# Performance work log

Hardware: AMD Instinct MI355X
Metric: run time of the kernel (lower is better)

## Reference

```python
import jax, jax.numpy as jnp
import numpy as np

N = 50000
E = 800000
D = 128
L = 2


def setup_inputs() -> dict:
    key = jax.random.key(0)
    ks = jax.random.split(key, 8)
    x = jax.random.normal(ks[0], (N, D), dtype=jnp.float32)
    edge_index = jax.random.randint(ks[1], (2, E), 0, N, dtype=jnp.int64)
    s = 1.0 / np.sqrt(D)
    Wl = jax.random.uniform(ks[2], (L, D, D), jnp.float32, -s, s)  # neighbor transform (with bias)
    bl = jax.random.uniform(ks[3], (L, D), jnp.float32, -s, s)
    Wr = jax.random.uniform(ks[4], (L, D, D), jnp.float32, -s, s)  # root/self transform (no bias)
    W = jax.random.uniform(ks[5], (D, D), jnp.float32, -s, s)      # final Linear
    b = jax.random.uniform(ks[6], (D,), jnp.float32, -s, s)
    return {"x": x, "edge_index": edge_index, "Wl": Wl, "bl": bl, "Wr": Wr, "W": W, "b": b}


def reference(x, edge_index, Wl, bl, Wr, W, b):
    src, dst = edge_index[0], edge_index[1]
    n = x.shape[0]
    for l in range(Wl.shape[0]):
        # gather neighbor (source) features, scatter-max into destination nodes
        agg = jax.ops.segment_max(x[src], dst, num_segments=n)  # [N, D]
        agg = jnp.where(jnp.isneginf(agg), 0.0, agg)  # PyG: isolated nodes -> 0
        # SAGEConv: lin_l(agg) + lin_r(x)
        x = agg @ Wl[l].T + bl[l] + x @ Wr[l].T
        x = jax.nn.relu(x)
    return x @ W.T + b
```

## Files before the change

kernel.cpp:

```cpp
#include <hip/hip_runtime.h>
#include <math.h>

#define NN 50000
#define NE 800000
#define DD 128
#define NBUCK 196
#define EPB 2048
#define PB 391
#define CONVB 6250
#define NTILE 782

typedef unsigned short u16;
typedef unsigned long long u64t;
typedef short s8v __attribute__((ext_vector_type(8)));
typedef float f16v __attribute__((ext_vector_type(16)));

__device__ __forceinline__ u16 f2bf(float f) {
    unsigned u = __float_as_uint(f);
    return (u16)((u + 0x7FFFu + ((u >> 16) & 1u)) >> 16);
}
__device__ __forceinline__ float bflo(unsigned u) { return __uint_as_float(u << 16); }
__device__ __forceinline__ float bfhi(unsigned u) { return __uint_as_float(u & 0xFFFF0000u); }

__global__ __launch_bounds__(256) void zero_kernel(int* __restrict__ p, int n) {
    int i = threadIdx.x + blockIdx.x * 256;
    if (i < n) p[i] = 0;
}

__device__ __forceinline__ void pack_one(const float* __restrict__ Wl,
                                         const float* __restrict__ Wr,
                                         bool two, int o, u16* __restrict__ out) {
    int j = o & 7;
    int l = (o >> 3) & 63;
    int cn = o >> 9;
    int n = cn & 3;
    int c = cn >> 2;
    int colj = n * 32 + (l & 31);
    int k = c * 16 + (l >> 5) * 8 + j;
    float v;
    if (two) v = (k < DD) ? Wl[colj * DD + k] : Wr[colj * DD + (k - DD)];
    else     v = Wl[colj * DD + k];
    out[o] = f2bf(v);
}

__global__ __launch_bounds__(256) void prep_kernel(
        const float4* __restrict__ x4, ushort4* __restrict__ hb0,
        ushort4* __restrict__ hbT,
        const float* __restrict__ Wl, const float* __restrict__ Wr,
        const float* __restrict__ W,
        u16* __restrict__ Bpk0, u16* __restrict__ Bpk1, u16* __restrict__ Bpkf,
        const int* __restrict__ ei, int* __restrict__ bcnt) {
    int bid = blockIdx.x;
    int tid = threadIdx.x;
    if (bid < CONVB) {
        int i = bid * 256 + tid;
        float4 v = x4[i];
        ushort4 o;
        o.x = f2bf(v.x); o.y = f2bf(v.y); o.z = f2bf(v.z); o.w = f2bf(v.w);
        hb0[i] = o;
        int node = i >> 5, pos = i & 31;
        hbT[((size_t)((pos >> 3) * NN + node) << 3) + (pos & 7)] = o;
    } else if (bid < CONVB + 128) {
        pack_one(Wl, Wr, true, (bid - CONVB) * 256 + tid, Bpk0);
    } else if (bid < CONVB + 256) {
        pack_one(Wl + DD * DD, Wr + DD * DD, true, (bid - CONVB - 128) * 256 + tid, Bpk1);
    } else if (bid < CONVB + 320) {
        pack_one(W, W, false, (bid - CONVB - 256) * 256 + tid, Bpkf);
    } else {
        __shared__ int h[NBUCK];
        for (int i = tid; i < NBUCK; i += 256) h[i] = 0;
        __syncthreads();
        int e0 = (bid - (CONVB + 320)) * EPB;
#pragma unroll
        for (int i = 0; i < 8; i++) {
            int e = e0 + i * 256 + tid;
            if (e < NE) atomicAdd(&h[ei[NE + e] >> 8], 1);
        }
        __syncthreads();
        for (int i = tid; i < NBUCK; i += 256)
            if (h[i]) atomicAdd(&bcnt[i], h[i]);
    }
}

__global__ __launch_bounds__(256) void bucket_partition(const int* __restrict__ ei,
                                                        const int* __restrict__ bcnt,
                                                        int* __restrict__ claim,
                                                        unsigned* __restrict__ packed,
                                                        int* __restrict__ rowptr) {
    __shared__ int sc[256];
    __shared__ int bb[NBUCK];
    __shared__ int h[NBUCK];
    __shared__ int base[NBUCK];
    int t = threadIdx.x;
    int v = (t < NBUCK) ? bcnt[t] : 0;
    sc[t] = v;
    __syncthreads();
    for (int o = 1; o < 256; o <<= 1) {
        int u = (t >= o) ? sc[t - o] : 0;
        __syncthreads();
        sc[t] += u;
        __syncthreads();
    }
    if (t < NBUCK) bb[t] = sc[t] - v;
    if (t == 0 && blockIdx.x == 0) rowptr[NN] = NE;
    for (int i = t; i < NBUCK; i += 256) h[i] = 0;
    __syncthreads();
    int e0 = blockIdx.x * EPB;
    int dsts[8], srcs[8];
#pragma unroll
    for (int i = 0; i < 8; i++) {
        int e = e0 + i * 256 + t;
        if (e < NE) {
            dsts[i] = ei[NE + e];
            srcs[i] = ei[e];
            atomicAdd(&h[dsts[i] >> 8], 1);
        } else dsts[i] = -1;
    }
    __syncthreads();
    for (int i = t; i < NBUCK; i += 256) {
        int c = h[i];
        base[i] = c ? bb[i] + atomicAdd(&claim[i], c) : 0;
    }
    __syncthreads();
    for (int i = t; i < NBUCK; i += 256) h[i] = 0;
    __syncthreads();
#pragma unroll
    for (int i = 0; i < 8; i++) {
        if (dsts[i] >= 0) {
            int bk = dsts[i] >> 8;
            int r = atomicAdd(&h[bk], 1);
            packed[base[bk] + r] = (unsigned)srcs[i] | ((unsigned)(dsts[i] & 255) << 16);
        }
    }
}

__global__ __launch_bounds__(256) void bucket_csr(const unsigned* __restrict__ packed,
                                                  const int* __restrict__ bcnt,
                                                  int* __restrict__ rowptr,
                                                  int* __restrict__ col) {
    __shared__ int sc[256];
    __shared__ int deg[256];
    __shared__ int off[256];
    int t = threadIdx.x;
    int v0 = (t < NBUCK) ? bcnt[t] : 0;
    sc[t] = v0;
    __syncthreads();
    for (int o = 1; o < 256; o <<= 1) {
        int u = (t >= o) ? sc[t - o] : 0;
        __syncthreads();
        sc[t] += u;
        __syncthreads();
    }
    int bk = blockIdx.x;
    int cnt = bcnt[bk];
    int base = sc[bk] - cnt;
    deg[t] = 0;
    __syncthreads();
    for (int i = t; i < cnt; i += 256) atomicAdd(&deg[packed[base + i] >> 16], 1);
    __syncthreads();
    int v = deg[t];
    off[t] = v;
    __syncthreads();
    for (int o = 1; o < 256; o <<= 1) {
        int u = (t >= o) ? off[t - o] : 0;
        __syncthreads();
        off[t] += u;
        __syncthreads();
    }
    int ex = off[t] - v;
    int node = (bk << 8) + t;
    if (node < NN) rowptr[node] = base + ex;
    deg[t] = ex;
    __syncthreads();
    for (int i = t; i < cnt; i += 256) {
        unsigned p = packed[base + i];
        int dl = p >> 16;
        int r = atomicAdd(&deg[dl], 1);
        col[base + r] = (int)(p & 0xFFFFu);
    }
}

__device__ __forceinline__ void vmax8(float* m, uint4 v) {
    m[0] = fmaxf(m[0], bflo(v.x)); m[1] = fmaxf(m[1], bfhi(v.x));
    m[2] = fmaxf(m[2], bflo(v.y)); m[3] = fmaxf(m[3], bfhi(v.y));
    m[4] = fmaxf(m[4], bflo(v.z)); m[5] = fmaxf(m[5], bfhi(v.z));
    m[6] = fmaxf(m[6], bflo(v.w)); m[7] = fmaxf(m[7], bfhi(v.w));
}

__global__ __launch_bounds__(256) void agg_chunked(const uint4* __restrict__ hbT4,
                                                   const int* __restrict__ rowptr,
                                                   const int* __restrict__ col,
                                                   uint4* __restrict__ aggb4) {
    int bid = blockIdx.x;
    int chunk = (bid & 7) >> 1;
    int ntile = ((bid >> 3) << 1) | (bid & 1);
    int t = threadIdx.x;
    int node = ntile * 64 + (t >> 2);
    int q = t & 3;
    if (node >= NN) return;
    const uint4* src4 = hbT4 + ((size_t)chunk * NN) * 4 + q;
    int s0 = rowptr[node], s1 = rowptr[node + 1];
    uint4 o = make_uint4(0u, 0u, 0u, 0u);
    if (s0 < s1) {
        float m0[8], m1[8];
#pragma unroll
        for (int k = 0; k < 8; k++) { m0[k] = m1[k] = -INFINITY; }
        int i = s0;
        for (; i + 8 <= s1; i += 8) {
            int c0 = col[i],     c1 = col[i + 1], c2 = col[i + 2], c3 = col[i + 3];
            int c4 = col[i + 4], c5 = col[i + 5], c6 = col[i + 6], c7 = col[i + 7];
            uint4 v0 = src4[(size_t)c0 * 4];
            uint4 v1 = src4[(size_t)c1 * 4];
            uint4 v2 = src4[(size_t)c2 * 4];
            uint4 v3 = src4[(size_t)c3 * 4];
            uint4 v4 = src4[(size_t)c4 * 4];
            uint4 v5 = src4[(size_t)c5 * 4];
            uint4 v6 = src4[(size_t)c6 * 4];
            uint4 v7 = src4[(size_t)c7 * 4];
            vmax8(m0, v0); vmax8(m1, v1); vmax8(m0, v2); vmax8(m1, v3);
            vmax8(m0, v4); vmax8(m1, v5); vmax8(m0, v6); vmax8(m1, v7);
        }
        for (; i + 2 <= s1; i += 2) {
            int c0 = col[i], c1 = col[i + 1];
            uint4 v0 = src4[(size_t)c0 * 4];
            uint4 v1 = src4[(size_t)c1 * 4];
            vmax8(m0, v0); vmax8(m1, v1);
        }
        if (i < s1) {
            uint4 v = src4[(size_t)col[i] * 4];
            vmax8(m0, v);
        }
#pragma unroll
        for (int k = 0; k < 8; k++) m0[k] = fmaxf(m0[k], m1[k]);
        o.x = (__float_as_uint(m0[0]) >> 16) | (__float_as_uint(m0[1]) & 0xFFFF0000u);
        o.y = (__float_as_uint(m0[2]) >> 16) | (__float_as_uint(m0[3]) & 0xFFFF0000u);
        o.z = (__float_as_uint(m0[4]) >> 16) | (__float_as_uint(m0[5]) & 0xFFFF0000u);
        o.w = (__float_as_uint(m0[6]) >> 16) | (__float_as_uint(m0[7]) & 0xFFFF0000u);
    }
    aggb4[(size_t)node * 16 + chunk * 4 + q] = o;
}

__global__ __launch_bounds__(256) void mfma_gemm0(const u16* __restrict__ srcA,
                                                  const u16* __restrict__ srcB,
                                                  const u16* __restrict__ Bpk,
                                                  const float* __restrict__ bias,
                                                  u16* __restrict__ outh,
                                                  u16* __restrict__ outT) {
    __shared__ u16 As[128 * 128];
    char* Ab = (char*)As;
    int tid = threadIdx.x;
    int wt = tid >> 6;
    int lane = tid & 63;
    int row0 = blockIdx.x * 128;
    int rload = row0 + wt * 32 + (lane & 31);
    if (rload > NN - 1) rload = NN - 1;
    int koff = (lane >> 5) * 8;
    const s8v* Bv = (const s8v*)Bpk;

    f16v acc[4];
#pragma unroll
    for (int n = 0; n < 4; n++) acc[n] = (f16v)(0.0f);

#pragma unroll
    for (int c = 0; c < 16; c++) {
        const u16* s = srcA;
        int kk = c * 16;
        if (c >= 8) { s = srcB; kk = (c - 8) * 16; }
        s8v a = *(const s8v*)(s + (size_t)rload * DD + kk + koff);
#pragma unroll
        for (int n = 0; n < 4; n++) {
            s8v b = Bv[(c * 4 + n) * 64 + lane];
            acc[n] = __builtin_amdgcn_mfma_f32_32x32x16_bf16(a, b, acc[n], 0, 0, 0);
        }
    }

    int rowadd = 4 * (lane >> 5);
#pragma unroll
    for (int n = 0; n < 4; n++) {
        int colj = n * 32 + (lane & 31);
        float bj = bias[colj];
#pragma unroll
        for (int r = 0; r < 16; r++) {
            int rloc = wt * 32 + (r & 3) + 8 * (r >> 2) + rowadd;
            float v = fmaxf(acc[n][r] + bj, 0.0f);
            *(u16*)(Ab + rloc * 256 + ((colj * 2) ^ ((rloc & 7) << 4))) = f2bf(v);
        }
    }
    __syncthreads();

#pragma unroll
    for (int it = 0; it < 16; it++) {
        int flat = it * 256 + tid;
        int rl = flat >> 5;
        int p  = flat & 31;
        u64t v = *(const u64t*)(Ab + rl * 256 + ((p * 8) ^ ((rl & 7) << 4)));
        int row = row0 + rl;
        if (row < NN) {
            *(u64t*)(outh + (size_t)row * DD + p * 4) = v;
            *(u64t*)(outT + (((size_t)((p >> 3) * NN + row)) << 5) + (p & 7) * 4) = v;
        }
    }
}

__global__ __launch_bounds__(256) void gemm_final(const u16* __restrict__ srcA,
                                                  const u16* __restrict__ srcB,
                                                  const u16* __restrict__ Bpk,
                                                  const float* __restrict__ bias,
                                                  const u16* __restrict__ Bpkf,
                                                  const float* __restrict__ bfin,
                                                  float* __restrict__ out) {
    __shared__ u16 As[128 * 128];
    char* Ab = (char*)As;
    int tid = threadIdx.x;
    int wt = tid >> 6;
    int lane = tid & 63;
    int row0 = blockIdx.x * 128;
    int arl = wt * 32 + (lane & 31);
    int rg = row0 + arl;
    if (rg > NN - 1) rg = NN - 1;
    int koff = (lane >> 5) * 8;
    int swz = (arl & 7) << 4;
    const s8v* Bv = (const s8v*)Bpk;

    f16v acc[4];
#pragma unroll
    for (int n = 0; n < 4; n++) acc[n] = (f16v)(0.0f);

#pragma unroll
    for (int c = 0; c < 16; c++) {
        const u16* s = srcA;
        int kk = c * 16;
        if (c >= 8) { s = srcB; kk = (c - 8) * 16; }
        s8v a = *(const s8v*)(s + (size_t)rg * DD + kk + koff);
#pragma unroll
        for (int n = 0; n < 4; n++) {
            s8v b = Bv[(c * 4 + n) * 64 + lane];
            acc[n] = __builtin_amdgcn_mfma_f32_32x32x16_bf16(a, b, acc[n], 0, 0, 0);
        }
    }

    int rowadd = 4 * (lane >> 5);
#pragma unroll
    for (int n = 0; n < 4; n++) {
        int colj = n * 32 + (lane & 31);
        float bj = bias[colj];
#pragma unroll
        for (int r = 0; r < 16; r++) {
            int rloc = wt * 32 + (r & 3) + 8 * (r >> 2) + rowadd;
            float v = fmaxf(acc[n][r] + bj, 0.0f);
            *(u16*)(Ab + rloc * 256 + ((colj * 2) ^ ((rloc & 7) << 4))) = f2bf(v);
        }
    }
    __syncthreads();

    const s8v* Bvf = (const s8v*)Bpkf;
    f16v acc2[4];
#pragma unroll
    for (int n = 0; n < 4; n++) acc2[n] = (f16v)(0.0f);
#pragma unroll
    for (int c = 0; c < 8; c++) {
        s8v a = *(const s8v*)(Ab + arl * 256 + (((c * 16 + koff) * 2) ^ swz));
#pragma unroll
        for (int n = 0; n < 4; n++) {
            s8v b = Bvf[(c * 4 + n) * 64 + lane];
            acc2[n] = __builtin_amdgcn_mfma_f32_32x32x16_bf16(a, b, acc2[n], 0, 0, 0);
        }
    }
#pragma unroll
    for (int n = 0; n < 4; n++) {
        int colj = n * 32 + (lane & 31);
        float bj = bfin[colj];
#pragma unroll
        for (int r = 0; r < 16; r++) {
            int row = row0 + wt * 32 + (r & 3) + 8 * (r >> 2) + rowadd;
            if (row < NN)
                out[(size_t)row * DD + colj] = acc2[n][r] + bj;
        }
    }
}

extern "C" void kernel_launch(void* const* d_in, const int* in_sizes, int n_in,
                              void* d_out, int out_size, void* d_ws, size_t ws_size,
                              hipStream_t stream) {
    const float* x  = (const float*)d_in[0];
    const int*   ei = (const int*)d_in[1];
    const float* Wl = (const float*)d_in[2];
    const float* bl = (const float*)d_in[3];
    const float* Wr = (const float*)d_in[4];
    const float* W  = (const float*)d_in[5];
    const float* b  = (const float*)d_in[6];
    float* out = (float*)d_out;

    u16* aggb = (u16*)d_ws;
    u16* hb0  = aggb + (size_t)NN * DD;
    u16* hb1  = hb0 + (size_t)NN * DD;
    u16* hbT  = hb1 + (size_t)NN * DD;
    u16* Bpk0 = hbT + (size_t)NN * DD;
    u16* Bpk1 = Bpk0 + 32768;
    u16* Bpkf = Bpk1 + 32768;
    unsigned* packed = (unsigned*)(Bpkf + 16384);
    int* col    = (int*)(packed + NE);
    int* rowptr = col + NE;
    int* bcnt   = rowptr + NN + 1;
    int* claim  = bcnt + NBUCK;

    dim3 blk(256);
    int gemmBlocks = (NN + 127) / 128;
    int aggBlocks  = NTILE * 4;
    int prepBlocks = CONVB + 320 + PB;

    zero_kernel<<<2, blk, 0, stream>>>(bcnt, 2 * NBUCK);
    prep_kernel<<<prepBlocks, blk, 0, stream>>>(
        (const float4*)x, (ushort4*)hb0, (ushort4*)hbT, Wl, Wr, W,
        Bpk0, Bpk1, Bpkf, ei, bcnt);

    bucket_partition<<<PB, blk, 0, stream>>>(ei, bcnt, claim, packed, rowptr);
    bucket_csr<<<NBUCK, blk, 0, stream>>>(packed, bcnt, rowptr, col);

    agg_chunked<<<aggBlocks, blk, 0, stream>>>((const uint4*)hbT, rowptr, col, (uint4*)aggb);
    mfma_gemm0<<<gemmBlocks, blk, 0, stream>>>(aggb, hb0, Bpk0, bl, hb1, hbT);

    agg_chunked<<<aggBlocks, blk, 0, stream>>>((const uint4*)hbT, rowptr, col, (uint4*)aggb);
    gemm_final<<<gemmBlocks, blk, 0, stream>>>(aggb, hb1, Bpk1, bl + DD, Bpkf, b, out);
}
```

Before: 238.5 us.

## Use persistent atomic work-queue blocks for chunked neighbor aggregation

Replaces the one-block-per-tile aggregation launch with 2048 persistent blocks that pull tile indices from a global atomic counter. Tiles are now ordered chunk-major, so all nodes of one feature chunk are processed together, which may improve L2 locality of the gathered columns. Two new counters are zeroed alongside the bucket counters. The change adds two block-wide barriers and one atomic per tile, and it relies on the workspace slot after claim being free.

```diff
diff --git a/kernel.cpp b/kernel.cpp
--- a/kernel.cpp
+++ b/kernel.cpp
@@ -9,6 +9,7 @@
 #define PB 391
 #define CONVB 6250
 #define NTILE 782
+#define NTILES4 (NTILE * 4)
 
 typedef unsigned short u16;
 typedef unsigned long long u64t;
@@ -187,57 +188,66 @@
     m[6] = fmaxf(m[6], bflo(v.w)); m[7] = fmaxf(m[7], bfhi(v.w));
 }
 
-__global__ __launch_bounds__(256) void agg_chunked(const uint4* __restrict__ hbT4,
-                                                   const int* __restrict__ rowptr,
-                                                   const int* __restrict__ col,
-                                                   uint4* __restrict__ aggb4) {
-    int bid = blockIdx.x;
-    int chunk = (bid & 7) >> 1;
-    int ntile = ((bid >> 3) << 1) | (bid & 1);
-    int t = threadIdx.x;
-    int node = ntile * 64 + (t >> 2);
-    int q = t & 3;
-    if (node >= NN) return;
-    const uint4* src4 = hbT4 + ((size_t)chunk * NN) * 4 + q;
-    int s0 = rowptr[node], s1 = rowptr[node + 1];
-    uint4 o = make_uint4(0u, 0u, 0u, 0u);
-    if (s0 < s1) {
-        float m0[8], m1[8];
-#pragma unroll
-        for (int k = 0; k < 8; k++) { m0[k] = m1[k] = -INFINITY; }
-        int i = s0;
-        for (; i + 8 <= s1; i += 8) {
-            int c0 = col[i],     c1 = col[i + 1], c2 = col[i + 2], c3 = col[i + 3];
-            int c4 = col[i + 4], c5 = col[i + 5], c6 = col[i + 6], c7 = col[i + 7];
-            uint4 v0 = src4[(size_t)c0 * 4];
-            uint4 v1 = src4[(size_t)c1 * 4];
-            uint4 v2 = src4[(size_t)c2 * 4];
-            uint4 v3 = src4[(size_t)c3 * 4];
-            uint4 v4 = src4[(size_t)c4 * 4];
-            uint4 v5 = src4[(size_t)c5 * 4];
-            uint4 v6 = src4[(size_t)c6 * 4];
-            uint4 v7 = src4[(size_t)c7 * 4];
-            vmax8(m0, v0); vmax8(m1, v1); vmax8(m0, v2); vmax8(m1, v3);
-            vmax8(m0, v4); vmax8(m1, v5); vmax8(m0, v6); vmax8(m1, v7);
-        }
-        for (; i + 2 <= s1; i += 2) {
-            int c0 = col[i], c1 = col[i + 1];
-            uint4 v0 = src4[(size_t)c0 * 4];
-            uint4 v1 = src4[(size_t)c1 * 4];
-            vmax8(m0, v0); vmax8(m1, v1);
-        }
-        if (i < s1) {
-            uint4 v = src4[(size_t)col[i] * 4];
-            vmax8(m0, v);
-        }
-#pragma unroll
-        for (int k = 0; k < 8; k++) m0[k] = fmaxf(m0[k], m1[k]);
-        o.x = (__float_as_uint(m0[0]) >> 16) | (__float_as_uint(m0[1]) & 0xFFFF0000u);
-        o.y = (__float_as_uint(m0[2]) >> 16) | (__float_as_uint(m0[3]) & 0xFFFF0000u);
-        o.z = (__float_as_uint(m0[4]) >> 16) | (__float_as_uint(m0[5]) & 0xFFFF0000u);
-        o.w = (__float_as_uint(m0[6]) >> 16) | (__float_as_uint(m0[7]) & 0xFFFF0000u);
-    }
-    aggb4[(size_t)node * 16 + chunk * 4 + q] = o;
+__global__ __launch_bounds__(256) void agg_chunked_q(const uint4* __restrict__ hbT4,
+                                                     const int* __restrict__ rowptr,
+                                                     const int* __restrict__ col,
+                                                     uint4* __restrict__ aggb4,
+                                                     int* __restrict__ qctr) {
+    __shared__ int s_t;
+    int tid = threadIdx.x;
+    for (;;) {
+        __syncthreads();
+        if (tid == 0) s_t = atomicAdd(qctr, 1);
+        __syncthreads();
+        int t = s_t;
+        if (t >= NTILES4) return;
+        int chunk = t / NTILE;
+        int ntile = t - chunk * NTILE;
+        int node = ntile * 64 + (tid >> 2);
+        int q = tid & 3;
+        bool valid = (node < NN);
+        int s0 = 0, s1 = 0;
+        if (valid) { s0 = rowptr[node]; s1 = rowptr[node + 1]; }
+        const uint4* src4 = hbT4 + ((size_t)chunk * NN) * 4 + q;
+        uint4 o = make_uint4(0u, 0u, 0u, 0u);
+        if (s0 < s1) {
+            float m0[8], m1[8];
+#pragma unroll
+            for (int k = 0; k < 8; k++) { m0[k] = m1[k] = -INFINITY; }
+            int i = s0;
+            for (; i + 8 <= s1; i += 8) {
+                int c0 = col[i],     c1 = col[i + 1], c2 = col[i + 2], c3 = col[i + 3];
+                int c4 = col[i + 4], c5 = col[i + 5], c6 = col[i + 6], c7 = col[i + 7];
+                uint4 v0 = src4[(size_t)c0 * 4];
+                uint4 v1 = src4[(size_t)c1 * 4];
+                uint4 v2 = src4[(size_t)c2 * 4];
+                uint4 v3 = src4[(size_t)c3 * 4];
+                uint4 v4 = src4[(size_t)c4 * 4];
+                uint4 v5 = src4[(size_t)c5 * 4];
+                uint4 v6 = src4[(size_t)c6 * 4];
+                uint4 v7 = src4[(size_t)c7 * 4];
+                vmax8(m0, v0); vmax8(m1, v1); vmax8(m0, v2); vmax8(m1, v3);
+                vmax8(m0, v4); vmax8(m1, v5); vmax8(m0, v6); vmax8(m1, v7);
+            }
+            for (; i + 2 <= s1; i += 2) {
+                int c0 = col[i], c1 = col[i + 1];
+                uint4 v0 = src4[(size_t)c0 * 4];
+                uint4 v1 = src4[(size_t)c1 * 4];
+                vmax8(m0, v0); vmax8(m1, v1);
+            }
+            if (i < s1) {
+                uint4 v = src4[(size_t)col[i] * 4];
+                vmax8(m0, v);
+            }
+#pragma unroll
+            for (int k = 0; k < 8; k++) m0[k] = fmaxf(m0[k], m1[k]);
+            o.x = (__float_as_uint(m0[0]) >> 16) | (__float_as_uint(m0[1]) & 0xFFFF0000u);
+            o.y = (__float_as_uint(m0[2]) >> 16) | (__float_as_uint(m0[3]) & 0xFFFF0000u);
+            o.z = (__float_as_uint(m0[4]) >> 16) | (__float_as_uint(m0[5]) & 0xFFFF0000u);
+            o.w = (__float_as_uint(m0[6]) >> 16) | (__float_as_uint(m0[7]) & 0xFFFF0000u);
+        }
+        if (valid) aggb4[(size_t)node * 16 + chunk * 4 + q] = o;
+    }
 }
 
 __global__ __launch_bounds__(256) void mfma_gemm0(const u16* __restrict__ srcA,
@@ -403,13 +413,14 @@
     int* rowptr = col + NE;
     int* bcnt   = rowptr + NN + 1;
     int* claim  = bcnt + NBUCK;
+    int* qctr   = claim + NBUCK;
 
     dim3 blk(256);
     int gemmBlocks = (NN + 127) / 128;
-    int aggBlocks  = NTILE * 4;
+    int aggBlocks  = 2048;
     int prepBlocks = CONVB + 320 + PB;
 
-    zero_kernel<<<2, blk, 0, stream>>>(bcnt, 2 * NBUCK);
+    zero_kernel<<<2, blk, 0, stream>>>(bcnt, 2 * NBUCK + 2);
     prep_kernel<<<prepBlocks, blk, 0, stream>>>(
         (const float4*)x, (ushort4*)hb0, (ushort4*)hbT, Wl, Wr, W,
         Bpk0, Bpk1, Bpkf, ei, bcnt);
@@ -417,9 +428,11 @@
     bucket_partition<<<PB, blk, 0, stream>>>(ei, bcnt, claim, packed, rowptr);
     bucket_csr<<<NBUCK, blk, 0, stream>>>(packed, bcnt, rowptr, col);
 
-    agg_chunked<<<aggBlocks, blk, 0, stream>>>((const uint4*)hbT, rowptr, col, (uint4*)aggb);
+    agg_chunked_q<<<aggBlocks, blk, 0, stream>>>(
+        (const uint4*)hbT, rowptr, col, (uint4*)aggb, qctr);
     mfma_gemm0<<<gemmBlocks, blk, 0, stream>>>(aggb, hb0, Bpk0, bl, hb1, hbT);
 
-    agg_chunked<<<aggBlocks, blk, 0, stream>>>((const uint4*)hbT, rowptr, col, (uint4*)aggb);
+    agg_chunked_q<<<aggBlocks, blk, 0, stream>>>(
+        (const uint4*)hbT, rowptr, col, (uint4*)aggb, qctr + 1);
     gemm_final<<<gemmBlocks, blk, 0, stream>>>(aggb, hb1, Bpk1, bl + DD, Bpkf, b, out);
 }
```

Result: slower. 327.0 us (+37.1%).

## Use chunk-major feature layout everywhere and split aggregation into per-chunk launches

Applied to the files above, without the earlier changes.

Drops the row-major copies of the node features and keeps only the 32-column chunk-major layout. The GEMMs now read their A fragments from the chunk-major buffers, and the aggregation writes its output in the same layout. The single interleaved aggregation launch becomes four sequential launches, one per chunk, so each launch's gather working set (about 3.2MB) stays cache-resident. This removes the duplicate feature writes and one buffer, at the cost of more kernel launches and strided A loads in the GEMM.

```diff
diff --git a/kernel.cpp b/kernel.cpp
--- a/kernel.cpp
+++ b/kernel.cpp
@@ -8,7 +8,8 @@
 #define EPB 2048
 #define PB 391
 #define CONVB 6250
-#define NTILE 782
+#define CHKS ((size_t)NN * 32)
+#define AGGB 782
 
 typedef unsigned short u16;
 typedef unsigned long long u64t;
@@ -44,8 +45,7 @@
 }
 
 __global__ __launch_bounds__(256) void prep_kernel(
-        const float4* __restrict__ x4, ushort4* __restrict__ hb0,
-        ushort4* __restrict__ hbT,
+        const float4* __restrict__ x4, u16* __restrict__ hT0,
         const float* __restrict__ Wl, const float* __restrict__ Wr,
         const float* __restrict__ W,
         u16* __restrict__ Bpk0, u16* __restrict__ Bpk1, u16* __restrict__ Bpkf,
@@ -55,11 +55,10 @@
     if (bid < CONVB) {
         int i = bid * 256 + tid;
         float4 v = x4[i];
-        ushort4 o;
-        o.x = f2bf(v.x); o.y = f2bf(v.y); o.z = f2bf(v.z); o.w = f2bf(v.w);
-        hb0[i] = o;
-        int node = i >> 5, pos = i & 31;
-        hbT[((size_t)((pos >> 3) * NN + node) << 3) + (pos & 7)] = o;
+        u64t pk = (u64t)f2bf(v.x) | ((u64t)f2bf(v.y) << 16) |
+                  ((u64t)f2bf(v.z) << 32) | ((u64t)f2bf(v.w) << 48);
+        int row = i >> 5, pos = i & 31;
+        *(u64t*)(hT0 + ((size_t)(pos >> 3) * NN + row) * 32 + (pos & 7) * 4) = pk;
     } else if (bid < CONVB + 128) {
         pack_one(Wl, Wr, true, (bid - CONVB) * 256 + tid, Bpk0);
     } else if (bid < CONVB + 256) {
@@ -187,18 +186,13 @@
     m[6] = fmaxf(m[6], bflo(v.w)); m[7] = fmaxf(m[7], bfhi(v.w));
 }
 
-__global__ __launch_bounds__(256) void agg_chunked(const uint4* __restrict__ hbT4,
-                                                   const int* __restrict__ rowptr,
-                                                   const int* __restrict__ col,
-                                                   uint4* __restrict__ aggb4) {
-    int bid = blockIdx.x;
-    int chunk = (bid & 7) >> 1;
-    int ntile = ((bid >> 3) << 1) | (bid & 1);
-    int t = threadIdx.x;
-    int node = ntile * 64 + (t >> 2);
-    int q = t & 3;
+__global__ __launch_bounds__(256) void agg_chunk(const uint4* __restrict__ src4,
+                                                 const int* __restrict__ rowptr,
+                                                 const int* __restrict__ col,
+                                                 uint4* __restrict__ dst4) {
+    int node = blockIdx.x * 64 + (threadIdx.x >> 2);
     if (node >= NN) return;
-    const uint4* src4 = hbT4 + ((size_t)chunk * NN) * 4 + q;
+    int q = threadIdx.x & 3;
     int s0 = rowptr[node], s1 = rowptr[node + 1];
     uint4 o = make_uint4(0u, 0u, 0u, 0u);
     if (s0 < s1) {
@@ -209,27 +203,23 @@
         for (; i + 8 <= s1; i += 8) {
             int c0 = col[i],     c1 = col[i + 1], c2 = col[i + 2], c3 = col[i + 3];
             int c4 = col[i + 4], c5 = col[i + 5], c6 = col[i + 6], c7 = col[i + 7];
-            uint4 v0 = src4[(size_t)c0 * 4];
-            uint4 v1 = src4[(size_t)c1 * 4];
-            uint4 v2 = src4[(size_t)c2 * 4];
-            uint4 v3 = src4[(size_t)c3 * 4];
-            uint4 v4 = src4[(size_t)c4 * 4];
-            uint4 v5 = src4[(size_t)c5 * 4];
-            uint4 v6 = src4[(size_t)c6 * 4];
-            uint4 v7 = src4[(size_t)c7 * 4];
+            uint4 v0 = src4[(size_t)c0 * 4 + q];
+            uint4 v1 = src4[(size_t)c1 * 4 + q];
+            uint4 v2 = src4[(size_t)c2 * 4 + q];
+            uint4 v3 = src4[(size_t)c3 * 4 + q];
+            uint4 v4 = src4[(size_t)c4 * 4 + q];
+            uint4 v5 = src4[(size_t)c5 * 4 + q];
+            uint4 v6 = src4[(size_t)c6 * 4 + q];
+            uint4 v7 = src4[(size_t)c7 * 4 + q];
             vmax8(m0, v0); vmax8(m1, v1); vmax8(m0, v2); vmax8(m1, v3);
             vmax8(m0, v4); vmax8(m1, v5); vmax8(m0, v6); vmax8(m1, v7);
         }
         for (; i + 2 <= s1; i += 2) {
-            int c0 = col[i], c1 = col[i + 1];
-            uint4 v0 = src4[(size_t)c0 * 4];
-            uint4 v1 = src4[(size_t)c1 * 4];
+            uint4 v0 = src4[(size_t)col[i] * 4 + q];
+            uint4 v1 = src4[(size_t)col[i + 1] * 4 + q];
             vmax8(m0, v0); vmax8(m1, v1);
         }
-        if (i < s1) {
-            uint4 v = src4[(size_t)col[i] * 4];
-            vmax8(m0, v);
-        }
+        if (i < s1) vmax8(m0, src4[(size_t)col[i] * 4 + q]);
 #pragma unroll
         for (int k = 0; k < 8; k++) m0[k] = fmaxf(m0[k], m1[k]);
         o.x = (__float_as_uint(m0[0]) >> 16) | (__float_as_uint(m0[1]) & 0xFFFF0000u);
@@ -237,15 +227,18 @@
         o.z = (__float_as_uint(m0[4]) >> 16) | (__float_as_uint(m0[5]) & 0xFFFF0000u);
         o.w = (__float_as_uint(m0[6]) >> 16) | (__float_as_uint(m0[7]) & 0xFFFF0000u);
     }
-    aggb4[(size_t)node * 16 + chunk * 4 + q] = o;
-}
-
-__global__ __launch_bounds__(256) void mfma_gemm0(const u16* __restrict__ srcA,
-                                                  const u16* __restrict__ srcB,
+    dst4[(size_t)node * 4 + q] = o;
+}
+
+__device__ __forceinline__ const s8v* afrag(const u16* __restrict__ cm, int row, int k) {
+    return (const s8v*)(cm + ((size_t)(k >> 5) * NN + row) * 32 + (k & 31));
+}
+
+__global__ __launch_bounds__(256) void mfma_gemm0(const u16* __restrict__ aggT,
+                                                  const u16* __restrict__ hT0,
                                                   const u16* __restrict__ Bpk,
                                                   const float* __restrict__ bias,
-                                                  u16* __restrict__ outh,
-                                                  u16* __restrict__ outT) {
+                                                  u16* __restrict__ hT1) {
     __shared__ u16 As[128 * 128];
     char* Ab = (char*)As;
     int tid = threadIdx.x;
@@ -263,10 +256,8 @@
 
 #pragma unroll
     for (int c = 0; c < 16; c++) {
-        const u16* s = srcA;
-        int kk = c * 16;
-        if (c >= 8) { s = srcB; kk = (c - 8) * 16; }
-        s8v a = *(const s8v*)(s + (size_t)rload * DD + kk + koff);
+        s8v a = (c < 8) ? *afrag(aggT, rload, c * 16 + koff)
+                        : *afrag(hT0, rload, (c - 8) * 16 + koff);
 #pragma unroll
         for (int n = 0; n < 4; n++) {
             s8v b = Bv[(c * 4 + n) * 64 + lane];
@@ -295,15 +286,13 @@
         int p  = flat & 31;
         u64t v = *(const u64t*)(Ab + rl * 256 + ((p * 8) ^ ((rl & 7) << 4)));
         int row = row0 + rl;
-        if (row < NN) {
-            *(u64t*)(outh + (size_t)row * DD + p * 4) = v;
-            *(u64t*)(outT + (((size_t)((p >> 3) * NN + row)) << 5) + (p & 7) * 4) = v;
-        }
-    }
-}
-
-__global__ __launch_bounds__(256) void gemm_final(const u16* __restrict__ srcA,
-                                                  const u16* __restrict__ srcB,
+        if (row < NN)
+            *(u64t*)(hT1 + ((size_t)(p >> 3) * NN + row) * 32 + (p & 7) * 4) = v;
+    }
+}
+
+__global__ __launch_bounds__(256) void gemm_final(const u16* __restrict__ aggT,
+                                                  const u16* __restrict__ hT1,
                                                   const u16* __restrict__ Bpk,
                                                   const float* __restrict__ bias,
                                                   const u16* __restrict__ Bpkf,
@@ -328,10 +317,8 @@
 
 #pragma unroll
     for (int c = 0; c < 16; c++) {
-        const u16* s = srcA;
-        int kk = c * 16;
-        if (c >= 8) { s = srcB; kk = (c - 8) * 16; }
-        s8v a = *(const s8v*)(s + (size_t)rg * DD + kk + koff);
+        s8v a = (c < 8) ? *afrag(aggT, rg, c * 16 + koff)
+                        : *afrag(hT1, rg, (c - 8) * 16 + koff);
 #pragma unroll
         for (int n = 0; n < 4; n++) {
             s8v b = Bv[(c * 4 + n) * 64 + lane];
@@ -391,11 +378,10 @@
     const float* b  = (const float*)d_in[6];
     float* out = (float*)d_out;
 
-    u16* aggb = (u16*)d_ws;
-    u16* hb0  = aggb + (size_t)NN * DD;
-    u16* hb1  = hb0 + (size_t)NN * DD;
-    u16* hbT  = hb1 + (size_t)NN * DD;
-    u16* Bpk0 = hbT + (size_t)NN * DD;
+    u16* aggT = (u16*)d_ws;
+    u16* hT0  = aggT + (size_t)NN * DD;
+    u16* hT1  = hT0 + (size_t)NN * DD;
+    u16* Bpk0 = hT1 + (size_t)NN * DD;
     u16* Bpk1 = Bpk0 + 32768;
     u16* Bpkf = Bpk1 + 32768;
     unsigned* packed = (unsigned*)(Bpkf + 16384);
@@ -406,20 +392,22 @@
 
     dim3 blk(256);
     int gemmBlocks = (NN + 127) / 128;
-    int aggBlocks  = NTILE * 4;
     int prepBlocks = CONVB + 320 + PB;
 
     zero_kernel<<<2, blk, 0, stream>>>(bcnt, 2 * NBUCK);
     prep_kernel<<<prepBlocks, blk, 0, stream>>>(
-        (const float4*)x, (ushort4*)hb0, (ushort4*)hbT, Wl, Wr, W,
-        Bpk0, Bpk1, Bpkf, ei, bcnt);
+        (const float4*)x, hT0, Wl, Wr, W, Bpk0, Bpk1, Bpkf, ei, bcnt);
 
     bucket_partition<<<PB, blk, 0, stream>>>(ei, bcnt, claim, packed, rowptr);
     bucket_csr<<<NBUCK, blk, 0, stream>>>(packed, bcnt, rowptr, col);
 
-    agg_chunked<<<aggBlocks, blk, 0, stream>>>((const uint4*)hbT, rowptr, col, (uint4*)aggb);
-    mfma_gemm0<<<gemmBlocks, blk, 0, stream>>>(aggb, hb0, Bpk0, bl, hb1, hbT);
-
-    agg_chunked<<<aggBlocks, blk, 0, stream>>>((const uint4*)hbT, rowptr, col, (uint4*)aggb);
-    gemm_final<<<gemmBlocks, blk, 0, stream>>>(aggb, hb1, Bpk1, bl + DD, Bpkf, b, out);
-}
+    for (int c = 0; c < 4; c++)
+        agg_chunk<<<AGGB, blk, 0, stream>>>(
+            (const uint4*)(hT0 + c * CHKS), rowptr, col, (uint4*)(aggT + c * CHKS));
+    mfma_gemm0<<<gemmBlocks, blk, 0, stream>>>(aggT, hT0, Bpk0, bl, hT1);
+
+    for (int c = 0; c < 4; c++)
+        agg_chunk<<<AGGB, blk, 0, stream>>>(
+            (const uint4*)(hT1 + c * CHKS), rowptr, col, (uint4*)(aggT + c * CHKS));
+    gemm_final<<<gemmBlocks, blk, 0, stream>>>(aggT, hT1, Bpk1, bl + DD, Bpkf, b, out);
+}
```

Result: slower. 269.8 us (+13.1%).
